# Optimization experiments

Measured on AMD Instinct MI355X. Metric: run time of the kernel, lower is better.

## Reference

```python
import jax, jax.numpy as jnp
import numpy as np


def apply_rope(t, seq_len, d_head):
    # t: [B, H, S, d_head]; interleaved-pair RoPE matching the torch module
    inv_freq = 1.0 / (10000.0 ** (jnp.arange(0, d_head, 2, dtype=jnp.float32) / d_head))
    angles = jnp.arange(seq_len, dtype=jnp.float32)[:, None] * inv_freq[None, :]  # [S, d/2]
    sin = jnp.sin(angles)[None, None, :, :, None]  # broadcast over B, H, pair
    cos = jnp.cos(angles)[None, None, :, :, None]
    tr = t.reshape(*t.shape[:-1], -1, 2)  # [B, H, S, d/2, 2]
    rot = jnp.stack([-tr[..., 1], tr[..., 0]], axis=-1)
    out = tr * cos + rot * sin
    return out.reshape(t.shape)


def setup_inputs() -> dict:
    key = jax.random.key(0)
    ks = jax.random.split(key, 10)
    B, S, D, L = 8, 4096, 1024, 64
    s = 0.02
    return {
        "x": jax.random.normal(ks[0], (B, S, D), dtype=jnp.float32),
        "latents": jax.random.normal(ks[1], (L, D), dtype=jnp.float32),
        "q_w": jax.random.normal(ks[2], (D, D), dtype=jnp.float32) * s,
        "q_b": jax.random.normal(ks[3], (D,), dtype=jnp.float32) * s,
        "k_w": jax.random.normal(ks[4], (D, D), dtype=jnp.float32) * s,
        "k_b": jax.random.normal(ks[5], (D,), dtype=jnp.float32) * s,
        "v_w": jax.random.normal(ks[6], (D, D), dtype=jnp.float32) * s,
        "v_b": jax.random.normal(ks[7], (D,), dtype=jnp.float32) * s,
        "out_w": jax.random.normal(ks[8], (D, D), dtype=jnp.float32) * s,
        "out_b": jax.random.normal(ks[9], (D,), dtype=jnp.float32) * s,
    }


def reference(x, latents, q_w, q_b, k_w, k_b, v_w, v_b, out_w, out_b):
    B, S, D = x.shape
    H = 16
    dh = D // H
    L = latents.shape[0]

    # latent queries (shared across batch)
    lq = latents @ q_w.T + q_b                      # [L, D]
    lq = jnp.broadcast_to(lq[None], (B, L, D))
    k = x @ k_w.T + k_b                             # [B, S, D]
    v = x @ v_w.T + v_b

    lq = lq.reshape(B, L, H, dh).transpose(0, 2, 1, 3)   # [B, H, L, dh]
    k = k.reshape(B, S, H, dh).transpose(0, 2, 1, 3)     # [B, H, S, dh]
    v = v.reshape(B, S, H, dh).transpose(0, 2, 1, 3)

    lq = apply_rope(lq, L, dh)
    k = apply_rope(k, S, dh)

    scores = jnp.einsum('bhld,bhsd->bhls', lq, k) / jnp.sqrt(jnp.float32(dh))
    attn = jax.nn.softmax(scores, axis=-1)
    out = jnp.einsum('bhls,bhsd->bhld', attn, v)          # [B, H, L, dh]
    out = out.transpose(0, 2, 1, 3).reshape(B, L, D)
    return out @ out_w.T + out_b
```

## Files before the change

### kernel.cpp

```cpp
#include <hip/hip_runtime.h>
#include <hip/hip_bf16.h>
#include <math.h>


typedef __attribute__((ext_vector_type(8))) short bf16x8;
typedef __attribute__((ext_vector_type(4))) float f32x4;

#define MFMA16(a, b, c) __builtin_amdgcn_mfma_f32_16x16x32_bf16((a), (b), (c), 0, 0, 0)

__device__ __forceinline__ unsigned short f2bf(float f) {
  unsigned int u = __float_as_uint(f);
  u = (u + 0x7fffu + ((u >> 16) & 1u)) >> 16;
  return (unsigned short)u;
}

__device__ __forceinline__ void gload_lds16(const void* g, void* l) {
  __builtin_amdgcn_global_load_lds((const __attribute__((address_space(1))) void*)g,
                                   (__attribute__((address_space(3))) void*)l,
                                   16, 0, 0);
}

__global__ __launch_bounds__(256) void cast_f32_bf16(const float* __restrict__ in,
                                                     unsigned short* __restrict__ out,
                                                     int n4) {
  int i = blockIdx.x * 256 + threadIdx.x;
  const int stride = gridDim.x * 256;
  for (; i < n4; i += stride) {
    const float4 v = ((const float4*)in)[i];
    ushort4 o;
    o.x = f2bf(v.x); o.y = f2bf(v.y); o.z = f2bf(v.z); o.w = f2bf(v.w);
    ((ushort4*)out)[i] = o;
  }
}

__global__ __launch_bounds__(256) void rope_table_kernel(float2* __restrict__ cs) {
  const int id = blockIdx.x * 256 + threadIdx.x;
  const int s = id >> 5, p = id & 31;
  const float inv = exp2f(-(float)p * 0.41524100875f);
  const float ang = (float)s * inv;
  cs[id] = make_float2(cosf(ang), sinf(ang));
}

__global__ __launch_bounds__(256) void lq_mfma_kernel(
    const unsigned short* __restrict__ latbf, const unsigned short* __restrict__ qwbf,
    const float* __restrict__ qb, const float2* __restrict__ cs,
    unsigned short* __restrict__ lqbf) {
  __shared__ unsigned short As[64 * 64];
  __shared__ unsigned short Bs[128 * 64];
  const int tid = threadIdx.x;
  const int lane = tid & 63, w = tid >> 6;
  const int cl = lane & 15, g8 = (lane >> 4) * 8, g4 = (lane >> 4) * 4;
  const int n0 = (int)blockIdx.x * 128;
  f32x4 acc[4][2] = {};
  for (int ks = 0; ks < 16; ++ks) {
    const int k0 = ks * 64;
    if (ks) __syncthreads();
#pragma unroll
    for (int i = 0; i < 2; ++i) {
      const int e = i * 2048 + tid * 8;
      gload_lds16(latbf + (size_t)(e >> 6) * 1024 + k0 + (e & 63), &As[i * 2048 + w * 512]);
    }
#pragma unroll
    for (int i = 0; i < 4; ++i) {
      const int e = i * 2048 + tid * 8;
      gload_lds16(qwbf + (size_t)(n0 + (e >> 6)) * 1024 + k0 + (e & 63), &Bs[i * 2048 + w * 512]);
    }
    __syncthreads();
#pragma unroll
    for (int kk = 0; kk < 2; ++kk) {
      bf16x8 af[4], bfr[2];
#pragma unroll
      for (int t = 0; t < 4; ++t)
        af[t] = *(const bf16x8*)&As[(t * 16 + cl) * 64 + kk * 32 + g8];
#pragma unroll
      for (int t = 0; t < 2; ++t)
        bfr[t] = *(const bf16x8*)&Bs[(w * 32 + t * 16 + cl) * 64 + kk * 32 + g8];
#pragma unroll
      for (int i = 0; i < 4; ++i)
#pragma unroll
        for (int j = 0; j < 2; ++j)
          acc[i][j] = MFMA16(af[i], bfr[j], acc[i][j]);
    }
  }
#pragma unroll
  for (int i = 0; i < 4; ++i)
#pragma unroll
    for (int j = 0; j < 2; ++j) {
      const int colg = n0 + w * 32 + j * 16 + cl;
      const float bv = qb[colg];
      const int p = (colg & 63) >> 1;
#pragma unroll
      for (int r = 0; r < 4; ++r) {
        const int l = i * 16 + g4 + r;
        float v = acc[i][j][r] + bv;
        const float2 c2 = cs[l * 32 + p];
        const float other = __shfl_xor(v, 1);
        v = (colg & 1) ? fmaf(v, c2.x, other * c2.y) : fmaf(v, c2.x, -other * c2.y);
        lqbf[l * 1024 + colg] = f2bf(v * 0.125f);
      }
    }
}

__global__ __launch_bounds__(512, 2) void kv_proj_kernel(
    const unsigned short* __restrict__ xbf,
    const unsigned short* __restrict__ kwbf, const unsigned short* __restrict__ vwbf,
    const float* __restrict__ kb, const float* __restrict__ vb,
    const float2* __restrict__ cs,
    unsigned short* __restrict__ Kbf, unsigned short* __restrict__ Vbf) {
  __shared__ unsigned short lds[2][4][8192];
  const int tid = threadIdx.x;
  const int lane = tid & 63, w = tid >> 6;
  const int wm = w >> 2, wn = w & 3;
  const int cl = lane & 15, g8 = (lane >> 4) * 8, g4 = (lane >> 4) * 4;
  const int bid = (int)blockIdx.x;
  const int swz = (bid & 7) * 128 + (bid >> 3);
  const int m0 = (swz >> 3) * 256;
  const int n0 = (swz & 7) * 256;
  const bool isK = n0 < 1024;
  const unsigned short* wbf = isK ? kwbf : vwbf;
  const int nl = isK ? n0 : n0 - 1024;

  const int srow = tid >> 2;
  const int sg8 = (tid & 3) * 8;
  const unsigned short* srcA = xbf + (size_t)(m0 + srow) * 1024 + sg8;
  const unsigned short* srcB = wbf + (size_t)(nl + srow) * 1024 + sg8;
  const int ldso0 = w * 512;
  const int ldso1 = 4096 + w * 512;

#define STAGE_A(nb_, slot_, koff_) do {                                   \
    gload_lds16(srcA + (koff_), &lds[nb_][slot_][ldso0]);                 \
    gload_lds16(srcA + 131072 + (koff_), &lds[nb_][slot_][ldso1]); } while (0)
#define STAGE_B(nb_, slot_, koff_) do {                                   \
    gload_lds16(srcB + (koff_), &lds[nb_][slot_][ldso0]);                 \
    gload_lds16(srcB + 131072 + (koff_), &lds[nb_][slot_][ldso1]); } while (0)

  const int rdA = (wm * 128 + cl) * 32 + g8;
  const int rdB = (wn * 64 + cl) * 32 + g8;

  f32x4 acc[8][4] = {};

  STAGE_A(0, 0, 0);
  STAGE_B(0, 2, 0);
  STAGE_A(0, 1, 32);
  STAGE_B(0, 3, 32);

#pragma unroll 2
  for (int t = 0; t < 16; ++t) {
    const int cb = t & 1, nb = cb ^ 1;
    const int tn = (t < 15) ? t + 1 : 15;
    const int kn = tn * 64;
#pragma unroll
    for (int kk = 0; kk < 2; ++kk) {
      asm volatile("s_waitcnt vmcnt(4)" ::: "memory");
      __builtin_amdgcn_s_barrier();
      asm volatile("" ::: "memory");
      bf16x8 aF[4], bF[4];
#pragma unroll
      for (int x = 0; x < 4; ++x)
        aF[x] = *(const bf16x8*)&lds[cb][kk][rdA + x * 512];
#pragma unroll
      for (int x = 0; x < 4; ++x)
        bF[x] = *(const bf16x8*)&lds[cb][2 + kk][rdB + x * 512];
      STAGE_A(nb, kk, kn + kk * 32);
      __builtin_amdgcn_s_setprio(1);
#pragma unroll
      for (int mf = 0; mf < 4; ++mf)
#pragma unroll
        for (int nf = 0; nf < 4; ++nf)
          acc[mf][nf] = MFMA16(aF[mf], bF[nf], acc[mf][nf]);
      __builtin_amdgcn_s_setprio(0);
      bf16x8 aG[4];
#pragma unroll
      for (int x = 0; x < 4; ++x)
        aG[x] = *(const bf16x8*)&lds[cb][kk][rdA + (4 + x) * 512];
      STAGE_B(nb, 2 + kk, kn + kk * 32);
      __builtin_amdgcn_s_setprio(1);
#pragma unroll
      for (int mf = 0; mf < 4; ++mf)
#pragma unroll
        for (int nf = 0; nf < 4; ++nf)
          acc[4 + mf][nf] = MFMA16(aG[mf], bF[nf], acc[4 + mf][nf]);
      __builtin_amdgcn_s_setprio(0);
    }
  }
  asm volatile("s_waitcnt vmcnt(0)" ::: "memory");
#undef STAGE_A
#undef STAGE_B

  const float* bias = isK ? kb : vb;
  unsigned short* outp = isK ? Kbf : Vbf;
#pragma unroll
  for (int mf = 0; mf < 8; ++mf) {
#pragma unroll
    for (int nf = 0; nf < 4; ++nf) {
      const int colg = nl + wn * 64 + nf * 16 + cl;
      const float bv = bias[colg];
#pragma unroll
      for (int r = 0; r < 4; ++r) {
        const int m = m0 + wm * 128 + mf * 16 + g4 + r;
        float v = acc[mf][nf][r] + bv;
        if (isK) {
          const int s = m & 4095;
          const int p = (colg & 63) >> 1;
          const float2 c2 = cs[s * 32 + p];
          const float other = __shfl_xor(v, 1);
          v = (colg & 1) ? fmaf(v, c2.x, other * c2.y) : fmaf(v, c2.x, -other * c2.y);
        }
        outp[(size_t)m * 1024 + colg] = f2bf(v);
      }
    }
  }
}

__global__ __launch_bounds__(256) void attn_kernel(
    const unsigned short* __restrict__ lqbf,
    const unsigned short* __restrict__ Kbf, const unsigned short* __restrict__ Vbf,
    float* __restrict__ Opart, float* __restrict__ ml) {
  __shared__ unsigned short Qs[64 * 64];
  __shared__ unsigned short Ks[4][32 * 64];
  __shared__ unsigned short Vs[4][32 * 64];
  __shared__ unsigned short Pb[4][64 * 32];
  const int tid = threadIdx.x;
  const int w = tid >> 6, lane = tid & 63;
  const int cl = lane & 15, g = lane >> 4, g8 = g * 8, g4 = g * 4;
  const int gid = blockIdx.x;
  const int c = gid & 3;
  const int h = (gid >> 2) & 15;
  const int b = gid >> 6;

#pragma unroll
  for (int i = 0; i < 2; ++i) {
    const int e = i * 2048 + tid * 8;
    const int l = e >> 6, d = e & 63;
    *(uint4*)&Qs[e] = *(const uint4*)&lqbf[l * 1024 + h * 64 + d];
  }
  __syncthreads();
  bf16x8 qf[4][2];
#pragma unroll
  for (int li = 0; li < 4; ++li)
#pragma unroll
    for (int kk = 0; kk < 2; ++kk)
      qf[li][kk] = *(const bf16x8*)&Qs[(li * 16 + cl) * 64 + kk * 32 + g8];

  float m_r[4][4], l_r[4][4];
  f32x4 acc_o[4][4] = {};
#pragma unroll
  for (int li = 0; li < 4; ++li)
#pragma unroll
    for (int r = 0; r < 4; ++r) { m_r[li][r] = -INFINITY; l_r[li][r] = 0.f; }

  const size_t kvbase = ((size_t)(b * 4096)) * 1024 + h * 64;
  for (int t = 0; t < 8; ++t) {
    const int s0 = c * 1024 + t * 128 + w * 32;
#pragma unroll
    for (int i = 0; i < 4; ++i) {
      const int e = i * 512 + lane * 8;
      const int r = e >> 6, d = e & 63;
      const size_t ga = kvbase + (size_t)(s0 + r) * 1024 + d;
      *(uint4*)&Ks[w][e] = *(const uint4*)&Kbf[ga];
      *(uint4*)&Vs[w][e] = *(const uint4*)&Vbf[ga];
    }
    f32x4 sc[4][2] = {};
#pragma unroll
    for (int kk = 0; kk < 2; ++kk)
#pragma unroll
      for (int sj = 0; sj < 2; ++sj) {
        const bf16x8 kf = *(const bf16x8*)&Ks[w][(sj * 16 + cl) * 64 + kk * 32 + g8];
#pragma unroll
        for (int li = 0; li < 4; ++li)
          sc[li][sj] = MFMA16(qf[li][kk], kf, sc[li][sj]);
      }
#pragma unroll
    for (int li = 0; li < 4; ++li) {
#pragma unroll
      for (int r = 0; r < 4; ++r) {
        const float v0 = sc[li][0][r], v1 = sc[li][1][r];
        float mx = fmaxf(v0, v1);
        mx = fmaxf(mx, __shfl_xor(mx, 1));
        mx = fmaxf(mx, __shfl_xor(mx, 2));
        mx = fmaxf(mx, __shfl_xor(mx, 4));
        mx = fmaxf(mx, __shfl_xor(mx, 8));
        const float mo = m_r[li][r];
        const float nm = fmaxf(mo, mx);
        const float p0 = __expf(v0 - nm);
        const float p1 = __expf(v1 - nm);
        const float f = __expf(mo - nm);
        m_r[li][r] = nm;
        float sp = p0 + p1;
        sp += __shfl_xor(sp, 1);
        sp += __shfl_xor(sp, 2);
        sp += __shfl_xor(sp, 4);
        sp += __shfl_xor(sp, 8);
        l_r[li][r] = l_r[li][r] * f + sp;
#pragma unroll
        for (int di = 0; di < 4; ++di) acc_o[li][di][r] *= f;
        const int lrow = li * 16 + g4 + r;
        Pb[w][lrow * 32 + cl] = f2bf(p0);
        Pb[w][lrow * 32 + 16 + cl] = f2bf(p1);
      }
    }
    bf16x8 pa[4];
#pragma unroll
    for (int li = 0; li < 4; ++li)
      pa[li] = *(const bf16x8*)&Pb[w][(li * 16 + cl) * 32 + g8];
#pragma unroll
    for (int di = 0; di < 4; ++di) {
      bf16x8 bv;
#pragma unroll
      for (int e = 0; e < 8; ++e)
        bv[e] = (short)Vs[w][(g8 + e) * 64 + di * 16 + cl];
#pragma unroll
      for (int li = 0; li < 4; ++li)
        acc_o[li][di] = MFMA16(pa[li], bv, acc_o[li][di]);
    }
  }
  const int part = c * 4 + w;
  const size_t obase = (((size_t)(b * 16 + h)) * 16 + part) * 4096;
#pragma unroll
  for (int li = 0; li < 4; ++li)
#pragma unroll
    for (int di = 0; di < 4; ++di)
#pragma unroll
      for (int r = 0; r < 4; ++r)
        Opart[obase + (size_t)(li * 16 + g4 + r) * 64 + di * 16 + cl] = acc_o[li][di][r];
  if (cl == 0) {
    const size_t mb = (((size_t)(b * 16 + h)) * 16 + part) * 128;
#pragma unroll
    for (int li = 0; li < 4; ++li)
#pragma unroll
      for (int r = 0; r < 4; ++r) {
        ml[mb + li * 16 + g4 + r] = m_r[li][r];
        ml[mb + 64 + li * 16 + g4 + r] = l_r[li][r];
      }
  }
}

__global__ __launch_bounds__(256) void combine_kernel(
    const float* __restrict__ Opart, const float* __restrict__ ml,
    float* __restrict__ attn_out) {
  const int id = blockIdx.x * 256 + threadIdx.x;
  const int d = id & 63;
  const int l = (id >> 6) & 63;
  const int h = (id >> 12) & 15;
  const int b = id >> 16;
  const size_t bh = (size_t)(b * 16 + h);
  float M = -INFINITY;
#pragma unroll
  for (int p = 0; p < 16; ++p) M = fmaxf(M, ml[(bh * 16 + p) * 128 + l]);
  float t = 0.f, acc = 0.f;
#pragma unroll
  for (int p = 0; p < 16; ++p) {
    const float mp = ml[(bh * 16 + p) * 128 + l];
    const float lp = ml[(bh * 16 + p) * 128 + 64 + l];
    const float wgt = __expf(mp - M);
    t += lp * wgt;
    acc += wgt * Opart[(bh * 16 + p) * 4096 + l * 64 + d];
  }
  attn_out[((size_t)(b * 64 + l)) * 1024 + h * 64 + d] = acc / t;
}

__global__ __launch_bounds__(256) void out_proj_kernel(
    const float* __restrict__ A, const float* __restrict__ Wt,
    const float* __restrict__ bias, float* __restrict__ C) {
  __shared__ float As[32 * 33];
  __shared__ float Bs[64 * 33];
  const int tid = threadIdx.x;
  const int m0 = (int)(blockIdx.x & 15) * 32;
  const int n0 = (int)(blockIdx.x >> 4) * 64;
  const int r0 = (tid >> 4) * 2;
  const int c0 = (tid & 15) * 4;
  float acc[2][4] = {};
  for (int k0 = 0; k0 < 1024; k0 += 32) {
    if (k0) __syncthreads();
    {
      const int row = tid >> 3, col = (tid & 7) * 4;
      const float4 a4 = *(const float4*)&A[(size_t)(m0 + row) * 1024 + k0 + col];
      As[row * 33 + col] = a4.x; As[row * 33 + col + 1] = a4.y;
      As[row * 33 + col + 2] = a4.z; As[row * 33 + col + 3] = a4.w;
    }
#pragma unroll
    for (int i = 0; i < 2; ++i) {
      const int e = i * 1024 + tid * 4;
      const int row = e >> 5, col = e & 31;
      const float4 b4 = *(const float4*)&Wt[(size_t)(n0 + row) * 1024 + k0 + col];
      Bs[row * 33 + col] = b4.x; Bs[row * 33 + col + 1] = b4.y;
      Bs[row * 33 + col + 2] = b4.z; Bs[row * 33 + col + 3] = b4.w;
    }
    __syncthreads();
#pragma unroll
    for (int kk = 0; kk < 32; ++kk) {
      const float a0 = As[r0 * 33 + kk], a1 = As[(r0 + 1) * 33 + kk];
      float bv[4];
#pragma unroll
      for (int j = 0; j < 4; ++j) bv[j] = Bs[(c0 + j) * 33 + kk];
#pragma unroll
      for (int j = 0; j < 4; ++j) {
        acc[0][j] = fmaf(a0, bv[j], acc[0][j]);
        acc[1][j] = fmaf(a1, bv[j], acc[1][j]);
      }
    }
  }
#pragma unroll
  for (int i = 0; i < 2; ++i)
#pragma unroll
    for (int j = 0; j < 4; ++j)
      C[(size_t)(m0 + r0 + i) * 1024 + n0 + c0 + j] = acc[i][j] + bias[n0 + c0 + j];
}

extern "C" void kernel_launch(void* const* d_in, const int* in_sizes, int n_in,
                              void* d_out, int out_size, void* d_ws, size_t ws_size,
                              hipStream_t stream) {
  (void)in_sizes; (void)n_in; (void)out_size; (void)ws_size;
  const float* x = (const float*)d_in[0];
  const float* latents = (const float*)d_in[1];
  const float* q_w = (const float*)d_in[2];
  const float* q_b = (const float*)d_in[3];
  const float* k_w = (const float*)d_in[4];
  const float* k_b = (const float*)d_in[5];
  const float* v_w = (const float*)d_in[6];
  const float* v_b = (const float*)d_in[7];
  const float* out_w = (const float*)d_in[8];
  const float* out_b = (const float*)d_in[9];
  float* out = (float*)d_out;

  char* ws = (char*)d_ws;
  size_t off = 0;
  auto alloc = [&](size_t bytes) {
    char* p = ws + off;
    off += (bytes + 255) & ~(size_t)255;
    return p;
  };
  unsigned short* xbf   = (unsigned short*)alloc(33554432ull * 2);
  unsigned short* kwbf  = (unsigned short*)alloc(1048576ull * 2);
  unsigned short* vwbf  = (unsigned short*)alloc(1048576ull * 2);
  unsigned short* qwbf  = (unsigned short*)alloc(1048576ull * 2);
  unsigned short* latbf = (unsigned short*)alloc(65536ull * 2);
  unsigned short* lqbf  = (unsigned short*)alloc(65536ull * 2);
  float2*         cs    = (float2*)alloc(4096ull * 32 * 8);
  unsigned short* Kbf   = (unsigned short*)alloc(33554432ull * 2);
  unsigned short* Vbf   = (unsigned short*)alloc(33554432ull * 2);
  float*          Opart = (float*)alloc(8ull * 16 * 16 * 4096 * 4);
  float*          mlbuf = (float*)alloc(8ull * 16 * 16 * 128 * 4);
  float*          attn_out = (float*)alloc(512ull * 1024 * 4);

  cast_f32_bf16<<<2048, 256, 0, stream>>>(x, xbf, 33554432 / 4);
  cast_f32_bf16<<<512, 256, 0, stream>>>(k_w, kwbf, 1048576 / 4);
  cast_f32_bf16<<<512, 256, 0, stream>>>(v_w, vwbf, 1048576 / 4);
  cast_f32_bf16<<<512, 256, 0, stream>>>(q_w, qwbf, 1048576 / 4);
  cast_f32_bf16<<<64, 256, 0, stream>>>(latents, latbf, 65536 / 4);
  rope_table_kernel<<<512, 256, 0, stream>>>(cs);
  lq_mfma_kernel<<<8, 256, 0, stream>>>(latbf, qwbf, q_b, cs, lqbf);
  kv_proj_kernel<<<1024, 512, 0, stream>>>(xbf, kwbf, vwbf, k_b, v_b, cs, Kbf, Vbf);
  attn_kernel<<<512, 256, 0, stream>>>(lqbf, Kbf, Vbf, Opart, mlbuf);
  combine_kernel<<<2048, 256, 0, stream>>>(Opart, mlbuf, attn_out);
  out_proj_kernel<<<256, 256, 0, stream>>>(attn_out, out_w, out_b, out);
}
```

Measured before the change: 590.3 us.

## Store V transposed, swizzle GEMM LDS staging, pad attention LDS tiles

The KV projection now writes V transposed as [D, B*S], so the attention kernel can load V^T rows into padded LDS and read MFMA B-fragments as single 16-byte vectors instead of eight scalar gathers. The GEMM main loop gets a new LDS layout with an XOR-style k-swizzle on staging and reads, plus a reorganised schedule with explicit barriers, lgkmcnt waits and two-tile-ahead prefetch. K, V^T and P tiles in attention are padded to cut LDS bank conflicts. In exchange, the transposed V stores are strided 8-byte writes, and the GEMM now has more barriers per iteration.

```diff
diff --git a/kernel.cpp b/kernel.cpp
--- a/kernel.cpp
+++ b/kernel.cpp
@@ -106,12 +106,12 @@
     const unsigned short* __restrict__ kwbf, const unsigned short* __restrict__ vwbf,
     const float* __restrict__ kb, const float* __restrict__ vb,
     const float2* __restrict__ cs,
-    unsigned short* __restrict__ Kbf, unsigned short* __restrict__ Vbf) {
-  __shared__ unsigned short lds[2][4][8192];
+    unsigned short* __restrict__ Kbf, unsigned short* __restrict__ VbfT) {
+  __shared__ unsigned short lds_u[2][2][2][8192];
   const int tid = threadIdx.x;
   const int lane = tid & 63, w = tid >> 6;
   const int wm = w >> 2, wn = w & 3;
-  const int cl = lane & 15, g8 = (lane >> 4) * 8, g4 = (lane >> 4) * 4;
+  const int cl = lane & 15, g4 = (lane >> 4) * 4;
   const int bid = (int)blockIdx.x;
   const int swz = (bid & 7) * 128 + (bid >> 3);
   const int m0 = (swz >> 3) * 256;
@@ -120,93 +120,107 @@
   const unsigned short* wbf = isK ? kwbf : vwbf;
   const int nl = isK ? n0 : n0 - 1024;
 
-  const int srow = tid >> 2;
-  const int sg8 = (tid & 3) * 8;
-  const unsigned short* srcA = xbf + (size_t)(m0 + srow) * 1024 + sg8;
-  const unsigned short* srcB = wbf + (size_t)(nl + srow) * 1024 + sg8;
-  const int ldso0 = w * 512;
-  const int ldso1 = 4096 + w * 512;
-
-#define STAGE_A(nb_, slot_, koff_) do {                                   \
-    gload_lds16(srcA + (koff_), &lds[nb_][slot_][ldso0]);                 \
-    gload_lds16(srcA + 131072 + (koff_), &lds[nb_][slot_][ldso1]); } while (0)
-#define STAGE_B(nb_, slot_, koff_) do {                                   \
-    gload_lds16(srcB + (koff_), &lds[nb_][slot_][ldso0]);                 \
-    gload_lds16(srcB + 131072 + (koff_), &lds[nb_][slot_][ldso1]); } while (0)
-
-  const int rdA = (wm * 128 + cl) * 32 + g8;
-  const int rdB = (wn * 64 + cl) * 32 + g8;
+  const int kswz = (((tid & 3) - ((tid >> 4) & 3)) & 3) * 8;
+  const unsigned short* srcA = xbf + (size_t)(m0 + (tid >> 2)) * 1024 + kswz;
+  const unsigned short* srcB = wbf + (size_t)(nl + (tid >> 2)) * 1024 + kswz;
+  const int wb = w * 512;
+
+  const int kA = (((lane >> 4) + (lane >> 2)) & 3) * 8;
+  const int rdA = (wm * 128 + cl) * 32 + kA;
+  const int rdB = (wn * 64 + cl) * 32 + kA;
+
+#define STG(db_, kh_, op_, kt_) do {                                          \
+    const unsigned short* s_ = (op_) ? srcB : srcA;                           \
+    unsigned short* d_ = &lds_u[db_][kh_][op_][wb];                           \
+    gload_lds16(s_ + (kt_) * 64 + (kh_) * 32, d_);                            \
+    gload_lds16(s_ + 131072 + (kt_) * 64 + (kh_) * 32, d_ + 4096); } while (0)
+
+#define BARX __builtin_amdgcn_s_barrier()
+#define LGKM0 asm volatile("s_waitcnt lgkmcnt(0)" ::: "memory")
+#define DS_A(cb_, kk_, mh_) do {                                              \
+    _Pragma("unroll") for (int x = 0; x < 4; ++x)                             \
+      aF[x] = *(const bf16x8*)&lds_u[cb_][kk_][0][rdA + (mh_) * 2048 + x * 512]; } while (0)
+#define DS_B(cb_, kk_) do {                                                   \
+    _Pragma("unroll") for (int x = 0; x < 4; ++x)                             \
+      bF[x] = *(const bf16x8*)&lds_u[cb_][kk_][1][rdB + x * 512]; } while (0)
+#define MMPH(mh_) do {                                                        \
+    __builtin_amdgcn_s_setprio(1);                                            \
+    _Pragma("unroll") for (int mf = 0; mf < 4; ++mf)                          \
+    _Pragma("unroll") for (int nf = 0; nf < 4; ++nf)                          \
+      acc[(mh_) * 4 + mf][nf] = MFMA16(aF[mf], bF[nf], acc[(mh_) * 4 + mf][nf]); \
+    __builtin_amdgcn_s_setprio(0); } while (0)
 
   f32x4 acc[8][4] = {};
 
-  STAGE_A(0, 0, 0);
-  STAGE_B(0, 2, 0);
-  STAGE_A(0, 1, 32);
-  STAGE_B(0, 3, 32);
+  STG(0, 0, 0, 0); STG(0, 0, 1, 0);
+  STG(0, 1, 0, 0); STG(0, 1, 1, 0);
+  STG(1, 0, 0, 1); STG(1, 0, 1, 1);
+  asm volatile("s_waitcnt vmcnt(4)" ::: "memory");
+  BARX;
 
 #pragma unroll 2
   for (int t = 0; t < 16; ++t) {
-    const int cb = t & 1, nb = cb ^ 1;
-    const int tn = (t < 15) ? t + 1 : 15;
-    const int kn = tn * 64;
-#pragma unroll
-    for (int kk = 0; kk < 2; ++kk) {
-      asm volatile("s_waitcnt vmcnt(4)" ::: "memory");
-      __builtin_amdgcn_s_barrier();
-      asm volatile("" ::: "memory");
-      bf16x8 aF[4], bF[4];
-#pragma unroll
-      for (int x = 0; x < 4; ++x)
-        aF[x] = *(const bf16x8*)&lds[cb][kk][rdA + x * 512];
-#pragma unroll
-      for (int x = 0; x < 4; ++x)
-        bF[x] = *(const bf16x8*)&lds[cb][2 + kk][rdB + x * 512];
-      STAGE_A(nb, kk, kn + kk * 32);
-      __builtin_amdgcn_s_setprio(1);
-#pragma unroll
-      for (int mf = 0; mf < 4; ++mf)
-#pragma unroll
-        for (int nf = 0; nf < 4; ++nf)
-          acc[mf][nf] = MFMA16(aF[mf], bF[nf], acc[mf][nf]);
-      __builtin_amdgcn_s_setprio(0);
-      bf16x8 aG[4];
-#pragma unroll
-      for (int x = 0; x < 4; ++x)
-        aG[x] = *(const bf16x8*)&lds[cb][kk][rdA + (4 + x) * 512];
-      STAGE_B(nb, 2 + kk, kn + kk * 32);
-      __builtin_amdgcn_s_setprio(1);
-#pragma unroll
-      for (int mf = 0; mf < 4; ++mf)
-#pragma unroll
-        for (int nf = 0; nf < 4; ++nf)
-          acc[4 + mf][nf] = MFMA16(aG[mf], bF[nf], acc[4 + mf][nf]);
-      __builtin_amdgcn_s_setprio(0);
-    }
+    const int cb = t & 1, ob = cb ^ 1;
+    const int u1 = (t < 15) ? t + 1 : 15;
+    const int u2 = (t < 14) ? t + 2 : 15;
+    bf16x8 aF[4], bF[4];
+    DS_B(cb, 0); DS_A(cb, 0, 0);
+    STG(ob, 1, 0, u1);
+    BARX; LGKM0; __builtin_amdgcn_sched_barrier(0);
+    MMPH(0);
+    BARX;
+    DS_A(cb, 0, 1);
+    STG(ob, 1, 1, u1);
+    BARX; LGKM0; __builtin_amdgcn_sched_barrier(0);
+    MMPH(1);
+    BARX;
+    DS_B(cb, 1); DS_A(cb, 1, 0);
+    STG(cb, 0, 0, u2);
+    BARX; LGKM0; __builtin_amdgcn_sched_barrier(0);
+    MMPH(0);
+    BARX;
+    DS_A(cb, 1, 1);
+    STG(cb, 0, 1, u2);
+    BARX; LGKM0; __builtin_amdgcn_sched_barrier(0);
+    MMPH(1);
+    asm volatile("s_waitcnt vmcnt(4)" ::: "memory");
+    BARX;
   }
   asm volatile("s_waitcnt vmcnt(0)" ::: "memory");
-#undef STAGE_A
-#undef STAGE_B
-
-  const float* bias = isK ? kb : vb;
-  unsigned short* outp = isK ? Kbf : Vbf;
+#undef STG
+#undef DS_A
+#undef DS_B
+#undef MMPH
+#undef BARX
+#undef LGKM0
+
 #pragma unroll
   for (int mf = 0; mf < 8; ++mf) {
 #pragma unroll
     for (int nf = 0; nf < 4; ++nf) {
       const int colg = nl + wn * 64 + nf * 16 + cl;
-      const float bv = bias[colg];
-#pragma unroll
-      for (int r = 0; r < 4; ++r) {
-        const int m = m0 + wm * 128 + mf * 16 + g4 + r;
-        float v = acc[mf][nf][r] + bv;
-        if (isK) {
+      if (isK) {
+        const float bv = kb[colg];
+#pragma unroll
+        for (int r = 0; r < 4; ++r) {
+          const int m = m0 + wm * 128 + mf * 16 + g4 + r;
+          float v = acc[mf][nf][r] + bv;
           const int s = m & 4095;
           const int p = (colg & 63) >> 1;
           const float2 c2 = cs[s * 32 + p];
           const float other = __shfl_xor(v, 1);
           v = (colg & 1) ? fmaf(v, c2.x, other * c2.y) : fmaf(v, c2.x, -other * c2.y);
+          Kbf[(size_t)m * 1024 + colg] = f2bf(v);
         }
-        outp[(size_t)m * 1024 + colg] = f2bf(v);
+      } else {
+        const float bv = vb[colg];
+        const int mb = m0 + wm * 128 + mf * 16 + g4;
+        ushort4 h4;
+        h4.x = f2bf(acc[mf][nf][0] + bv);
+        h4.y = f2bf(acc[mf][nf][1] + bv);
+        h4.z = f2bf(acc[mf][nf][2] + bv);
+        h4.w = f2bf(acc[mf][nf][3] + bv);
+        *(ushort4*)(VbfT + (size_t)colg * 32768 + mb) = h4;
       }
     }
   }
@@ -214,12 +228,12 @@
 
 __global__ __launch_bounds__(256) void attn_kernel(
     const unsigned short* __restrict__ lqbf,
-    const unsigned short* __restrict__ Kbf, const unsigned short* __restrict__ Vbf,
+    const unsigned short* __restrict__ Kbf, const unsigned short* __restrict__ VbfT,
     float* __restrict__ Opart, float* __restrict__ ml) {
   __shared__ unsigned short Qs[64 * 64];
-  __shared__ unsigned short Ks[4][32 * 64];
-  __shared__ unsigned short Vs[4][32 * 64];
-  __shared__ unsigned short Pb[4][64 * 32];
+  __shared__ unsigned short Ks[4][32 * 72];
+  __shared__ unsigned short VsT[4][64 * 40];
+  __shared__ unsigned short Pb[4][64 * 40];
   const int tid = threadIdx.x;
   const int w = tid >> 6, lane = tid & 63;
   const int cl = lane & 15, g = lane >> 4, g8 = g * 8, g4 = g * 4;
@@ -249,23 +263,24 @@
 #pragma unroll
     for (int r = 0; r < 4; ++r) { m_r[li][r] = -INFINITY; l_r[li][r] = 0.f; }
 
-  const size_t kvbase = ((size_t)(b * 4096)) * 1024 + h * 64;
+  const size_t kbase = ((size_t)(b * 4096)) * 1024 + h * 64;
+  const size_t vtbase = (size_t)(h * 64) * 32768 + (size_t)b * 4096;
   for (int t = 0; t < 8; ++t) {
     const int s0 = c * 1024 + t * 128 + w * 32;
 #pragma unroll
     for (int i = 0; i < 4; ++i) {
       const int e = i * 512 + lane * 8;
-      const int r = e >> 6, d = e & 63;
-      const size_t ga = kvbase + (size_t)(s0 + r) * 1024 + d;
-      *(uint4*)&Ks[w][e] = *(const uint4*)&Kbf[ga];
-      *(uint4*)&Vs[w][e] = *(const uint4*)&Vbf[ga];
+      *(uint4*)&Ks[w][(e >> 6) * 72 + (e & 63)] =
+          *(const uint4*)&Kbf[kbase + (size_t)(s0 + (e >> 6)) * 1024 + (e & 63)];
+      *(uint4*)&VsT[w][(e >> 5) * 40 + (e & 31)] =
+          *(const uint4*)&VbfT[vtbase + (size_t)(e >> 5) * 32768 + s0 + (e & 31)];
     }
     f32x4 sc[4][2] = {};
 #pragma unroll
     for (int kk = 0; kk < 2; ++kk)
 #pragma unroll
       for (int sj = 0; sj < 2; ++sj) {
-        const bf16x8 kf = *(const bf16x8*)&Ks[w][(sj * 16 + cl) * 64 + kk * 32 + g8];
+        const bf16x8 kf = *(const bf16x8*)&Ks[w][(sj * 16 + cl) * 72 + kk * 32 + g8];
 #pragma unroll
         for (int li = 0; li < 4; ++li)
           sc[li][sj] = MFMA16(qf[li][kk], kf, sc[li][sj]);
@@ -295,23 +310,20 @@
 #pragma unroll
         for (int di = 0; di < 4; ++di) acc_o[li][di][r] *= f;
         const int lrow = li * 16 + g4 + r;
-        Pb[w][lrow * 32 + cl] = f2bf(p0);
-        Pb[w][lrow * 32 + 16 + cl] = f2bf(p1);
+        Pb[w][lrow * 40 + cl] = f2bf(p0);
+        Pb[w][lrow * 40 + 16 + cl] = f2bf(p1);
       }
     }
     bf16x8 pa[4];
 #pragma unroll
     for (int li = 0; li < 4; ++li)
-      pa[li] = *(const bf16x8*)&Pb[w][(li * 16 + cl) * 32 + g8];
+      pa[li] = *(const bf16x8*)&Pb[w][(li * 16 + cl) * 40 + g8];
 #pragma unroll
     for (int di = 0; di < 4; ++di) {
-      bf16x8 bv;
-#pragma unroll
-      for (int e = 0; e < 8; ++e)
-        bv[e] = (short)Vs[w][(g8 + e) * 64 + di * 16 + cl];
+      const bf16x8 vv = *(const bf16x8*)&VsT[w][(di * 16 + cl) * 40 + g8];
 #pragma unroll
       for (int li = 0; li < 4; ++li)
-        acc_o[li][di] = MFMA16(pa[li], bv, acc_o[li][di]);
+        acc_o[li][di] = MFMA16(pa[li], vv, acc_o[li][di]);
     }
   }
   const int part = c * 4 + w;
@@ -438,7 +450,7 @@
   unsigned short* lqbf  = (unsigned short*)alloc(65536ull * 2);
   float2*         cs    = (float2*)alloc(4096ull * 32 * 8);
   unsigned short* Kbf   = (unsigned short*)alloc(33554432ull * 2);
-  unsigned short* Vbf   = (unsigned short*)alloc(33554432ull * 2);
+  unsigned short* VbfT  = (unsigned short*)alloc(33554432ull * 2);
   float*          Opart = (float*)alloc(8ull * 16 * 16 * 4096 * 4);
   float*          mlbuf = (float*)alloc(8ull * 16 * 16 * 128 * 4);
   float*          attn_out = (float*)alloc(512ull * 1024 * 4);
@@ -450,8 +462,8 @@
   cast_f32_bf16<<<64, 256, 0, stream>>>(latents, latbf, 65536 / 4);
   rope_table_kernel<<<512, 256, 0, stream>>>(cs);
   lq_mfma_kernel<<<8, 256, 0, stream>>>(latbf, qwbf, q_b, cs, lqbf);
-  kv_proj_kernel<<<1024, 512, 0, stream>>>(xbf, kwbf, vwbf, k_b, v_b, cs, Kbf, Vbf);
-  attn_kernel<<<512, 256, 0, stream>>>(lqbf, Kbf, Vbf, Opart, mlbuf);
+  kv_proj_kernel<<<1024, 512, 0, stream>>>(xbf, kwbf, vwbf, k_b, v_b, cs, Kbf, VbfT);
+  attn_kernel<<<512, 256, 0, stream>>>(lqbf, Kbf, VbfT, Opart, mlbuf);
   combine_kernel<<<2048, 256, 0, stream>>>(Opart, mlbuf, attn_out);
   out_proj_kernel<<<256, 256, 0, stream>>>(attn_out, out_w, out_b, out);
 }
```

New measurement: 603.0 us. +2.2%, slower.
